# Kernel optimization log

Hardware: AMD Instinct MI355X
Metric: run time of the kernel (lower is better)

## Reference

```python
import jax, jax.numpy as jnp
import numpy as np

R = 3            # num_relations
H = 256          # hid_dim
N0, N1, N2, N3 = 50000, 10000, 4000, 1024   # sampled node counts per hop
FAN = 16         # in-edges per target node
NB_NODES = 100000


def setup_inputs() -> dict:
    keys = iter(jax.random.split(jax.random.key(0), 80))
    def nrm(shape, scale=1.0):
        return jax.random.normal(next(keys), shape, jnp.float32) * scale
    inp = {}
    inp["features"] = nrm((NB_NODES, H))
    inp["n_ids"] = jax.random.randint(next(keys), (R, N0), 0, NB_NODES)
    def edges(n_src, n_dst):
        src = jax.random.randint(next(keys), (R, n_dst * FAN), 0, n_src)
        dst = jnp.tile(jnp.repeat(jnp.arange(n_dst), FAN)[None, :], (R, 1))
        return src, dst
    inp["src1"], inp["dst1"] = edges(N0, N1)
    inp["src2"], inp["dst2"] = edges(N1, N2)
    inp["src3"], inp["dst3"] = edges(N2, N3)
    def tconv_params(p, din, heads, ch):
        hc = heads * ch
        s = 1.0 / np.sqrt(din)
        for nm in ("Wq", "Wk", "Wv", "Ws"):
            inp[p + nm] = nrm((R, din, hc), s)
        for nm in ("bq", "bk", "bv", "bs"):
            inp[p + nm] = jnp.zeros((R, hc), jnp.float32)
        inp[p + "Wb"] = nrm((R, 3 * hc, 1), 1.0 / np.sqrt(3 * hc))
    tconv_params("l1_", H, 2, H // 2)
    tconv_params("l2_", H, 1, H // 2)
    tconv_params("l3_", H // 2, 1, H)
    inp["w_omega"] = nrm((H, H), 1.0 / np.sqrt(H))
    inp["b_omega"] = jnp.zeros((H,), jnp.float32)
    inp["u_omega"] = nrm((H,), 1.0 / np.sqrt(H))
    inp["rl"] = jnp.ones((R, 1), jnp.float32)
    return inp


def _tconv(x, src, dst, n_dst, P, heads, ch):
    """PyG TransformerConv with beta=True (gated skip), concat heads, eval mode."""
    Wq, bq, Wk, bk, Wv, bv, Ws, bs, Wb = P
    x_dst = x[:n_dst]
    q = (x_dst @ Wq + bq).reshape(n_dst, heads, ch)
    k = (x @ Wk + bk).reshape(-1, heads, ch)
    v = (x @ Wv + bv).reshape(-1, heads, ch)
    logit = (q[dst] * k[src]).sum(-1) * (1.0 / np.sqrt(ch))        # [E, heads]
    m = jax.ops.segment_max(logit, dst, num_segments=n_dst)
    p = jnp.exp(logit - m[dst])
    z = jax.ops.segment_sum(p, dst, num_segments=n_dst)
    a = p / z[dst]                                                  # edge softmax
    out = jax.ops.segment_sum(v[src] * a[..., None], dst, num_segments=n_dst)
    out = out.reshape(n_dst, heads * ch)
    x_r = x_dst @ Ws + bs
    g = jax.nn.sigmoid(jnp.concatenate([out, x_r, out - x_r], -1) @ Wb)
    return g * x_r + (1.0 - g) * out


def _rel_forward(feats, n_id, s1, d1, s2, d2, s3, d3, P1, P2, P3):
    x = feats[n_id]                                     # [N0, H]
    x = _tconv(x, s1, d1, N1, P1, 2, H // 2)            # [N1, H]
    x = (x - x.mean(0)) / jnp.sqrt(x.var(0) + 1e-5)     # BatchNorm1d (batch stats, identity affine)
    x = jax.nn.elu(x)
    x = _tconv(x, s2, d2, N2, P2, 1, H // 2)            # [N2, H/2]
    x = _tconv(x, s3, d3, N3, P3, 1, H)                 # [N3, H]
    return x


def _forward(features, n_ids, src1, dst1, src2, dst2, src3, dst3,
             l1_Wq, l1_bq, l1_Wk, l1_bk, l1_Wv, l1_bv, l1_Ws, l1_bs, l1_Wb,
             l2_Wq, l2_bq, l2_Wk, l2_bk, l2_Wv, l2_bv, l2_Ws, l2_bs, l2_Wb,
             l3_Wq, l3_bq, l3_Wk, l3_bk, l3_Wv, l3_bv, l3_Ws, l3_bs, l3_Wb,
             w_omega, b_omega, u_omega, rl):
    P1 = (l1_Wq, l1_bq, l1_Wk, l1_bk, l1_Wv, l1_bv, l1_Ws, l1_bs, l1_Wb)
    P2 = (l2_Wq, l2_bq, l2_Wk, l2_bk, l2_Wv, l2_bv, l2_Ws, l2_bs, l2_Wb)
    P3 = (l3_Wq, l3_bq, l3_Wk, l3_bk, l3_Wv, l3_bv, l3_Ws, l3_bs, l3_Wb)
    per_rel = jax.vmap(_rel_forward, in_axes=(None, 0, 0, 0, 0, 0, 0, 0, 0, 0, 0))
    emb = per_rel(features, n_ids, src1, dst1, src2, dst2, src3, dst3, P1, P2, P3)  # [R, N3, H]
    multi = emb.transpose(1, 0, 2) * rl[None]            # [N3, R, H], RL-threshold scaled
    v = jnp.tanh(multi @ w_omega + b_omega)              # [N3, R, H]
    alphas = jax.nn.softmax(v @ u_omega, axis=1)         # [N3, R]
    return (multi * alphas[..., None]).sum(1)            # [N3, H]


def reference(features, n_ids, src1, dst1, src2, dst2, src3, dst3,
              l1_Wq, l1_bq, l1_Wk, l1_bk, l1_Wv, l1_bv, l1_Ws, l1_bs, l1_Wb,
              l2_Wq, l2_bq, l2_Wk, l2_bk, l2_Wv, l2_bv, l2_Ws, l2_bs, l2_Wb,
              l3_Wq, l3_bq, l3_Wk, l3_bk, l3_Wv, l3_bv, l3_Ws, l3_bs, l3_Wb,
              w_omega, b_omega, u_omega, rl):
    return _forward(features, n_ids, src1, dst1, src2, dst2, src3, dst3,
                    l1_Wq, l1_bq, l1_Wk, l1_bk, l1_Wv, l1_bv, l1_Ws, l1_bs, l1_Wb,
                    l2_Wq, l2_bq, l2_Wk, l2_bk, l2_Wv, l2_bv, l2_Ws, l2_bs, l2_Wb,
                    l3_Wq, l3_bq, l3_Wk, l3_bk, l3_Wv, l3_bv, l3_Ws, l3_bs, l3_Wb,
                    w_omega, b_omega, u_omega, rl)
```

## Files before the change

kernel.cpp:

```cpp
#include <hip/hip_runtime.h>
#include <hip/hip_bf16.h>
#include <math.h>

#define H 256
#define N0 50000
#define N1 10000
#define N2 4000
#define N3 1024
#define FAN 16

typedef __hip_bfloat16 bf16;
typedef __attribute__((ext_vector_type(8))) short short8;
typedef __attribute__((ext_vector_type(4))) short short4v;
typedef __attribute__((ext_vector_type(2))) short short2v;
typedef __attribute__((ext_vector_type(4))) float floatx4;

typedef const __attribute__((address_space(1))) void* gas_ptr;
typedef __attribute__((address_space(3))) void* las_ptr;

__device__ __forceinline__ void load_lds16(const void* g, void* l) {
    __builtin_amdgcn_global_load_lds((gas_ptr)g, (las_ptr)l, 16, 0, 0);
}

__device__ __forceinline__ float2 cvt_bf2(unsigned u) {
    union { unsigned q; float f; } lo, hi;
    lo.q = u << 16; hi.q = u & 0xffff0000u;
    return make_float2(lo.f, hi.f);
}

template<int K>
__global__ __launch_bounds__(256, 4) void gemm_dual(
    const bf16* __restrict__ A, size_t Astr,
    const bf16* __restrict__ BtKV, const bf16* __restrict__ BtQS,
    const float* __restrict__ bk, const float* __restrict__ bv,
    const float* __restrict__ bq, const float* __restrict__ bs, int Nh,
    bf16* __restrict__ Ckv, size_t CkvStr, int Mkv,
    float* __restrict__ Cqs, size_t CqsStr, int Mqs,
    int nbKV)
{
    constexpr int KC = K / 32;
    constexpr int CPR = K / 8;
    constexpr int LOG_CPR = (K == 256) ? 5 : 4;
    constexpr int RPI = 64 / CPR;
    constexpr int ISSUES = 16 / RPI;
    const int N = 2 * Nh;
    __shared__ bf16 A_s[64 * K];

    const int z = blockIdx.z;
    const bool isKV = (int)blockIdx.x < nbKV;
    const int bx = isKV ? blockIdx.x : blockIdx.x - nbKV;
    const int M = isKV ? Mkv : Mqs;
    const bf16* Bt = (isKV ? BtKV : BtQS) + (size_t)z * N * K;
    const float* b1 = (isKV ? bk : bq) + (size_t)z * Nh;
    const float* b2 = (isKV ? bv : bs) + (size_t)z * Nh;
    A += (size_t)z * Astr;

    const int lane = threadIdx.x & 63;
    const int w = threadIdx.x >> 6;
    const int lm = lane & 15;
    const int q = lane >> 4;
    const int mbase = bx * 64;
    const int n0 = blockIdx.y * 256;

    {
        const int ch = lane & (CPR - 1);
        const int rsub = lane >> LOG_CPR;
        #pragma unroll
        for (int i = 0; i < ISSUES; i++) {
            int row = w * 16 + i * RPI + rsub;
            int grow = mbase + row; grow = grow < M ? grow : M - 1;
            int gch = ch ^ (row & 7);
            load_lds16(A + (size_t)grow * K + gch * 8,
                       A_s + (size_t)(w * 16 + i * RPI) * K);
        }
    }

    const bf16* bp[4];
    #pragma unroll
    for (int ni = 0; ni < 4; ni++)
        bp[ni] = Bt + (size_t)(n0 + w * 64 + ni * 16 + lm) * K + q * 8;

    floatx4 acc[4][4];
    #pragma unroll
    for (int i = 0; i < 4; i++)
        #pragma unroll
        for (int j = 0; j < 4; j++)
            acc[i][j] = (floatx4){0.f, 0.f, 0.f, 0.f};

    __syncthreads();

    short8 bn[4];
    #pragma unroll
    for (int ni = 0; ni < 4; ni++) bn[ni] = *(const short8*)(bp[ni]);

    #pragma unroll
    for (int kc = 0; kc < KC; kc++) {
        short8 bc[4];
        #pragma unroll
        for (int ni = 0; ni < 4; ni++) bc[ni] = bn[ni];
        if (kc + 1 < KC) {
            #pragma unroll
            for (int ni = 0; ni < 4; ni++)
                bn[ni] = *(const short8*)(bp[ni] + (kc + 1) * 32);
        }
        short8 af[4];
        #pragma unroll
        for (int mi = 0; mi < 4; mi++) {
            int row = mi * 16 + lm;
            af[mi] = *(const short8*)(A_s + row * K + (((kc * 4 + q) ^ (lm & 7)) * 8));
        }
        #pragma unroll
        for (int mi = 0; mi < 4; mi++)
            #pragma unroll
            for (int ni = 0; ni < 4; ni++)
                acc[mi][ni] = __builtin_amdgcn_mfma_f32_16x16x32_bf16(
                    af[mi], bc[ni], acc[mi][ni], 0, 0, 0);
    }

    if (isKV) {
        bf16* C = Ckv + (size_t)z * CkvStr;
        __syncthreads();
        bf16* stg = A_s + (size_t)w * (16 * 72);
        #pragma unroll
        for (int p = 0; p < 4; p++) {
            #pragma unroll
            for (int ni = 0; ni < 4; ni++) {
                int colg = n0 + w * 64 + ni * 16 + lm;
                float bias = (colg < Nh) ? b1[colg] : b2[colg - Nh];
                #pragma unroll
                for (int rg = 0; rg < 4; rg++)
                    stg[(q * 4 + rg) * 72 + ni * 16 + lm] = (bf16)(acc[p][ni][rg] + bias);
            }
            #pragma unroll
            for (int it = 0; it < 2; it++) {
                int rl = it * 8 + (lane >> 3);
                int grow = mbase + p * 16 + rl;
                short8 vv = *(const short8*)(stg + rl * 72 + (lane & 7) * 8);
                if (grow < M)
                    *(short8*)(C + (size_t)grow * N + n0 + w * 64 + (lane & 7) * 8) = vv;
            }
        }
    } else {
        float* C = Cqs + (size_t)z * CqsStr;
        #pragma unroll
        for (int ni = 0; ni < 4; ni++) {
            int colg = n0 + w * 64 + ni * 16 + lm;
            float bias = (colg < Nh) ? b1[colg] : b2[colg - Nh];
            #pragma unroll
            for (int mi = 0; mi < 4; mi++) {
                int rb = mbase + mi * 16 + q * 4;
                #pragma unroll
                for (int rg = 0; rg < 4; rg++) {
                    int rr = rb + rg;
                    if (rr < M) C[(size_t)rr * N + colg] = acc[mi][ni][rg] + bias;
                }
            }
        }
    }
}

__global__ __launch_bounds__(256) void gather_bf16(
    const float* __restrict__ F, const int* __restrict__ n_ids, bf16* __restrict__ out,
    int nrows)
{
    int z = blockIdx.y;
    const int* idx = n_ids + (size_t)z * nrows;
    bf16* o = out + (size_t)z * nrows * H;
    int t = blockIdx.x * 256 + threadIdx.x;
    int row = t >> 6;
    if (row >= nrows) return;
    int c4 = (t & 63) * 4;
    float4 v = *(const float4*)(F + (size_t)idx[row] * H + c4);
    bf16 tmp[4] = {(bf16)v.x, (bf16)v.y, (bf16)v.z, (bf16)v.w};
    *(short4v*)(o + (size_t)row * H + c4) = *(const short4v*)tmp;
}

__global__ __launch_bounds__(256) void pack_all(
    const float* __restrict__ l1_Wk, const float* __restrict__ l1_Wv,
    const float* __restrict__ l1_Wq, const float* __restrict__ l1_Ws,
    const float* __restrict__ l2_Wk, const float* __restrict__ l2_Wv,
    const float* __restrict__ l2_Wq, const float* __restrict__ l2_Ws,
    const float* __restrict__ l3_Wk, const float* __restrict__ l3_Wv,
    const float* __restrict__ l3_Wq, const float* __restrict__ l3_Ws,
    bf16* __restrict__ Wkv1, bf16* __restrict__ Wqs1,
    bf16* __restrict__ Wkv2, bf16* __restrict__ Wqs2,
    bf16* __restrict__ Wkv3, bf16* __restrict__ Wqs3)
{
    int job = blockIdx.z, r = blockIdx.y, nn = blockIdx.x, k = threadIdx.x;
    const float *W1, *W2; bf16* Wt; int K, Nh;
    switch (job) {
        case 0: W1 = l1_Wk; W2 = l1_Wv; Wt = Wkv1; K = 256; Nh = 256; break;
        case 1: W1 = l1_Wq; W2 = l1_Ws; Wt = Wqs1; K = 256; Nh = 256; break;
        case 2: W1 = l2_Wk; W2 = l2_Wv; Wt = Wkv2; K = 256; Nh = 128; break;
        case 3: W1 = l2_Wq; W2 = l2_Ws; Wt = Wqs2; K = 256; Nh = 128; break;
        case 4: W1 = l3_Wk; W2 = l3_Wv; Wt = Wkv3; K = 128; Nh = 256; break;
        default: W1 = l3_Wq; W2 = l3_Ws; Wt = Wqs3; K = 128; Nh = 256; break;
    }
    if (nn >= 2 * Nh || k >= K) return;
    size_t wstride = (size_t)K * Nh;
    float v = (nn < Nh) ? W1[(size_t)r * wstride + (size_t)k * Nh + nn]
                        : W2[(size_t)r * wstride + (size_t)k * Nh + (nn - Nh)];
    Wt[(size_t)r * 2 * wstride + (size_t)nn * K + k] = (bf16)v;
}

template<int CPL, int HEADS>
__global__ __launch_bounds__(256) void attn_gate(
    const float* __restrict__ qs, size_t qsStr,
    const bf16* __restrict__ kv, size_t kvStr,
    const int* __restrict__ src,
    const float* __restrict__ Wb,
    float* __restrict__ yf, size_t yfStr,
    bf16* __restrict__ yb, size_t ybStr,
    int ndst, float scale)
{
    constexpr int hc = CPL * 64;
    constexpr int LPH = 64 / HEADS;
    const int z = blockIdx.y;
    int lane = threadIdx.x & 63;
    int d = blockIdx.x * 4 + (threadIdx.x >> 6);
    if (d >= ndst) return;
    qs += (size_t)z * qsStr;
    kv += (size_t)z * kvStr;
    src += (size_t)z * ndst * FAN;
    Wb += (size_t)z * 3 * hc;

    const float* qp = qs + (size_t)d * (2 * hc) + lane * CPL;
    float qv[CPL], xv[CPL];
    if constexpr (CPL == 2) {
        float2 a = *(const float2*)qp;
        float2 b = *(const float2*)(qp + hc);
        qv[0] = a.x; qv[1] = a.y; xv[0] = b.x; xv[1] = b.y;
    } else {
        float4 a = *(const float4*)qp;
        float4 b = *(const float4*)(qp + hc);
        qv[0] = a.x; qv[1] = a.y; qv[2] = a.z; qv[3] = a.w;
        xv[0] = b.x; xv[1] = b.y; xv[2] = b.z; xv[3] = b.w;
    }
    const int* sp = src + (size_t)d * FAN;
    int sidx[FAN];
    #pragma unroll
    for (int e = 0; e < FAN; e++) sidx[e] = sp[e];

    float part[FAN];
    #pragma unroll
    for (int e = 0; e < FAN; e++) {
        const bf16* kp = kv + (size_t)sidx[e] * (2 * hc) + lane * CPL;
        if constexpr (CPL == 2) {
            float2 kf = cvt_bf2(*(const unsigned*)kp);
            part[e] = qv[0] * kf.x + qv[1] * kf.y;
        } else {
            uint2 u = *(const uint2*)kp;
            float2 k0 = cvt_bf2(u.x), k1 = cvt_bf2(u.y);
            part[e] = qv[0] * k0.x + qv[1] * k0.y + qv[2] * k1.x + qv[3] * k1.y;
        }
    }
    float logit[FAN], mx = -1e30f;
    #pragma unroll
    for (int e = 0; e < FAN; e++) {
        float dt = part[e];
        #pragma unroll
        for (int off = LPH / 2; off > 0; off >>= 1) dt += __shfl_xor(dt, off, 64);
        dt *= scale;
        logit[e] = dt;
        mx = fmaxf(mx, dt);
    }
    float zsum = 0.f, p[FAN];
    #pragma unroll
    for (int e = 0; e < FAN; e++) { p[e] = __expf(logit[e] - mx); zsum += p[e]; }
    float inv = 1.f / zsum;

    float ov[CPL];
    #pragma unroll
    for (int j = 0; j < CPL; j++) ov[j] = 0.f;
    #pragma unroll
    for (int e = 0; e < FAN; e++) {
        const bf16* vp = kv + (size_t)sidx[e] * (2 * hc) + hc + lane * CPL;
        if constexpr (CPL == 2) {
            float2 vf = cvt_bf2(*(const unsigned*)vp);
            ov[0] += p[e] * vf.x; ov[1] += p[e] * vf.y;
        } else {
            uint2 u = *(const uint2*)vp;
            float2 v0 = cvt_bf2(u.x), v1 = cvt_bf2(u.y);
            ov[0] += p[e] * v0.x; ov[1] += p[e] * v0.y;
            ov[2] += p[e] * v1.x; ov[3] += p[e] * v1.y;
        }
    }
    #pragma unroll
    for (int j = 0; j < CPL; j++) ov[j] *= inv;

    float s = 0.f;
    #pragma unroll
    for (int j = 0; j < CPL; j++) {
        int c = lane * CPL + j;
        s += ov[j] * Wb[c] + xv[j] * Wb[hc + c] + (ov[j] - xv[j]) * Wb[2 * hc + c];
    }
    #pragma unroll
    for (int off = 32; off > 0; off >>= 1) s += __shfl_xor(s, off, 64);
    float g = 1.f / (1.f + __expf(-s));

    float yv[CPL];
    #pragma unroll
    for (int j = 0; j < CPL; j++) yv[j] = g * xv[j] + (1.f - g) * ov[j];

    if (yf) {
        float* op = yf + (size_t)z * yfStr + (size_t)d * hc + lane * CPL;
        if constexpr (CPL == 2) *(float2*)op = make_float2(yv[0], yv[1]);
        else *(float4*)op = make_float4(yv[0], yv[1], yv[2], yv[3]);
    }
    if (yb) {
        bf16* op = yb + (size_t)z * ybStr + (size_t)d * hc + lane * CPL;
        bf16 tmp[CPL];
        #pragma unroll
        for (int j = 0; j < CPL; j++) tmp[j] = (bf16)yv[j];
        if constexpr (CPL == 2) *(short2v*)op = *(const short2v*)tmp;
        else *(short4v*)op = *(const short4v*)tmp;
    }
}

__global__ __launch_bounds__(256) void colstat_partial(
    const bf16* __restrict__ x, size_t xStr, int M,
    float* __restrict__ ps, float* __restrict__ pss)
{
    int z = blockIdx.y;
    const bf16* xp = x + (size_t)z * xStr;
    int f = threadIdx.x;
    int b = blockIdx.x;
    float s = 0.f, ss = 0.f;
    for (int r = b; r < M; r += 64) {
        float v = (float)xp[(size_t)r * H + f];
        s += v; ss += v * v;
    }
    ps[((size_t)z * 64 + b) * H + f] = s;
    pss[((size_t)z * 64 + b) * H + f] = ss;
}

__global__ __launch_bounds__(256) void colfinal_norm_elu(
    const float* __restrict__ ps, const float* __restrict__ pss,
    bf16* __restrict__ x, size_t xStr, int M)
{
    int z = blockIdx.y;
    bf16* xp = x + (size_t)z * xStr;
    int c = threadIdx.x;
    float s = 0.f, ss = 0.f;
    #pragma unroll 8
    for (int b = 0; b < 64; b++) {
        s += ps[((size_t)z * 64 + b) * H + c];
        ss += pss[((size_t)z * 64 + b) * H + c];
    }
    float mu = s / M;
    float istd = rsqrtf(ss / M - mu * mu + 1e-5f);
    for (int r = blockIdx.x; r < M; r += gridDim.x) {
        float t = ((float)xp[(size_t)r * H + c] - mu) * istd;
        xp[(size_t)r * H + c] = (bf16)(t > 0.f ? t : __expf(t) - 1.0f);
    }
}

__global__ __launch_bounds__(256) void semantic_kernel(
    const float* __restrict__ emb,
    const float* __restrict__ Wo, const float* __restrict__ bo,
    const float* __restrict__ uo, const float* __restrict__ rl,
    float* __restrict__ outp)
{
    __shared__ float m_s[3][H];
    __shared__ float red[H];
    __shared__ float score_s[3];
    int n = blockIdx.x, c = threadIdx.x;
    for (int r = 0; r < 3; r++)
        m_s[r][c] = emb[((size_t)r * N3 + n) * H + c] * rl[r];
    __syncthreads();
    for (int r = 0; r < 3; r++) {
        float t = bo[c];
        for (int k2 = 0; k2 < H; k2++) t += m_s[r][k2] * Wo[k2 * H + c];
        red[c] = tanhf(t) * uo[c];
        __syncthreads();
        for (int s = 128; s > 0; s >>= 1) {
            if (c < s) red[c] += red[c + s];
            __syncthreads();
        }
        if (c == 0) score_s[r] = red[0];
        __syncthreads();
    }
    float s0 = score_s[0], s1 = score_s[1], s2 = score_s[2];
    float mx = fmaxf(s0, fmaxf(s1, s2));
    float e0 = __expf(s0 - mx), e1 = __expf(s1 - mx), e2 = __expf(s2 - mx);
    float zi = 1.0f / (e0 + e1 + e2);
    outp[(size_t)n * H + c] = (m_s[0][c] * e0 + m_s[1][c] * e1 + m_s[2][c] * e2) * zi;
}

extern "C" void kernel_launch(void* const* d_in, const int* in_sizes, int n_in,
                              void* d_out, int out_size, void* d_ws, size_t ws_size,
                              hipStream_t stream) {
    const float* features = (const float*)d_in[0];
    const int*   n_ids    = (const int*)d_in[1];
    const int*   src1     = (const int*)d_in[2];
    const int*   src2     = (const int*)d_in[4];
    const int*   src3     = (const int*)d_in[6];
    const float* l1_Wq = (const float*)d_in[8];
    const float* l1_Wk = (const float*)d_in[9];
    const float* l1_Wv = (const float*)d_in[10];
    const float* l1_Ws = (const float*)d_in[11];
    const float* l1_bq = (const float*)d_in[12];
    const float* l1_bk = (const float*)d_in[13];
    const float* l1_bv = (const float*)d_in[14];
    const float* l1_bs = (const float*)d_in[15];
    const float* l1_Wb = (const float*)d_in[16];
    const float* l2_Wq = (const float*)d_in[17];
    const float* l2_Wk = (const float*)d_in[18];
    const float* l2_Wv = (const float*)d_in[19];
    const float* l2_Ws = (const float*)d_in[20];
    const float* l2_bq = (const float*)d_in[21];
    const float* l2_bk = (const float*)d_in[22];
    const float* l2_bv = (const float*)d_in[23];
    const float* l2_bs = (const float*)d_in[24];
    const float* l2_Wb = (const float*)d_in[25];
    const float* l3_Wq = (const float*)d_in[26];
    const float* l3_Wk = (const float*)d_in[27];
    const float* l3_Wv = (const float*)d_in[28];
    const float* l3_Ws = (const float*)d_in[29];
    const float* l3_bq = (const float*)d_in[30];
    const float* l3_bk = (const float*)d_in[31];
    const float* l3_bv = (const float*)d_in[32];
    const float* l3_bs = (const float*)d_in[33];
    const float* l3_Wb = (const float*)d_in[34];
    const float* w_omega = (const float*)d_in[35];
    const float* b_omega = (const float*)d_in[36];
    const float* u_omega = (const float*)d_in[37];
    const float* rl      = (const float*)d_in[38];

    float* ws = (float*)d_ws;
    size_t o = 0;
    float* emb = ws + o; o += (size_t)3 * N3 * H;
    float* qs1 = ws + o; o += (size_t)3 * N1 * 512;
    float* qs2 = ws + o; o += (size_t)3 * N2 * 256;
    float* qs3 = ws + o; o += (size_t)3 * N3 * 512;
    float* ps  = ws + o; o += (size_t)3 * 64 * H;
    float* pss = ws + o; o += (size_t)3 * 64 * H;

    bf16* bws = (bf16*)(ws + o);
    size_t b = 0;
    bf16* Xg  = bws + b; b += (size_t)3 * N0 * H;
    bf16* kv1 = bws + b; b += (size_t)3 * N0 * 512;
    bf16* x1b = bws + b; b += (size_t)3 * N1 * 256;
    bf16* kv2 = bws + b; b += (size_t)3 * N1 * 256;
    bf16* x2b = bws + b; b += (size_t)3 * N2 * 128;
    bf16* kv3 = bws + b; b += (size_t)3 * N2 * 512;
    bf16* Wkv1 = bws + b; b += (size_t)3 * 512 * H;
    bf16* Wqs1 = bws + b; b += (size_t)3 * 512 * H;
    bf16* Wkv2 = bws + b; b += (size_t)3 * 256 * H;
    bf16* Wqs2 = bws + b; b += (size_t)3 * 256 * H;
    bf16* Wkv3 = bws + b; b += (size_t)3 * 512 * 128;
    bf16* Wqs3 = bws + b; b += (size_t)3 * 512 * 128;

    const float sc128 = 0.088388347648318447f;
    const float sc256 = 0.0625f;

    pack_all<<<dim3(512, 3, 6), 256, 0, stream>>>(
        l1_Wk, l1_Wv, l1_Wq, l1_Ws, l2_Wk, l2_Wv, l2_Wq, l2_Ws,
        l3_Wk, l3_Wv, l3_Wq, l3_Ws, Wkv1, Wqs1, Wkv2, Wqs2, Wkv3, Wqs3);

    gather_bf16<<<dim3((N0 * 64 + 255) / 256, 3), 256, 0, stream>>>(
        features, n_ids, Xg, N0);

    {
        int nbKV = (N0 + 63) / 64, nbQS = (N1 + 63) / 64;
        gemm_dual<256><<<dim3(nbKV + nbQS, 2, 3), 256, 0, stream>>>(
            Xg, (size_t)N0 * H, Wkv1, Wqs1, l1_bk, l1_bv, l1_bq, l1_bs, 256,
            kv1, (size_t)N0 * 512, N0, qs1, (size_t)N1 * 512, N1, nbKV);
    }
    attn_gate<4, 2><<<dim3((N1 + 3) / 4, 3), 256, 0, stream>>>(
        qs1, (size_t)N1 * 512, kv1, (size_t)N0 * 512, src1, l1_Wb,
        (float*)nullptr, 0, x1b, (size_t)N1 * 256, N1, sc128);
    colstat_partial<<<dim3(64, 3), 256, 0, stream>>>(x1b, (size_t)N1 * 256, N1, ps, pss);
    colfinal_norm_elu<<<dim3(128, 3), 256, 0, stream>>>(ps, pss, x1b, (size_t)N1 * 256, N1);

    {
        int nbKV = (N1 + 63) / 64, nbQS = (N2 + 63) / 64;
        gemm_dual<256><<<dim3(nbKV + nbQS, 1, 3), 256, 0, stream>>>(
            x1b, (size_t)N1 * 256, Wkv2, Wqs2, l2_bk, l2_bv, l2_bq, l2_bs, 128,
            kv2, (size_t)N1 * 256, N1, qs2, (size_t)N2 * 256, N2, nbKV);
    }
    attn_gate<2, 1><<<dim3((N2 + 3) / 4, 3), 256, 0, stream>>>(
        qs2, (size_t)N2 * 256, kv2, (size_t)N1 * 256, src2, l2_Wb,
        (float*)nullptr, 0, x2b, (size_t)N2 * 128, N2, sc128);

    {
        int nbKV = (N2 + 63) / 64, nbQS = (N3 + 63) / 64;
        gemm_dual<128><<<dim3(nbKV + nbQS, 2, 3), 256, 0, stream>>>(
            x2b, (size_t)N2 * 128, Wkv3, Wqs3, l3_bk, l3_bv, l3_bq, l3_bs, 256,
            kv3, (size_t)N2 * 512, N2, qs3, (size_t)N3 * 512, N3, nbKV);
    }
    attn_gate<4, 1><<<dim3((N3 + 3) / 4, 3), 256, 0, stream>>>(
        qs3, (size_t)N3 * 512, kv3, (size_t)N2 * 512, src3, l3_Wb,
        emb, (size_t)N3 * H, (bf16*)nullptr, 0, N3, sc256);

    semantic_kernel<<<N3, 256, 0, stream>>>(emb, w_omega, b_omega, u_omega, rl, (float*)d_out);
}
```

Baseline: 614.7 us.

## Make dual GEMM persistent with double-buffered LDS prefetch of next A tile

The dual K/V and Q/S projection GEMM becomes a persistent kernel: a capped grid walks over row tiles in a stride loop, and the async global-to-LDS load of the next A tile is issued into a second LDS buffer while the current tile is computed. B fragments are also prefetched two k-steps ahead instead of one. The goal is to hide A-tile load latency and per-block launch and ramp-up cost. In exchange, LDS use doubles, the occupancy hint drops from 4 to 2 blocks per unit, and register pressure rises.

Result: no change. 613.0 us (-0.3%).

```diff
diff --git a/kernel.cpp b/kernel.cpp
--- a/kernel.cpp
+++ b/kernel.cpp
@@ -29,14 +29,14 @@
 }
 
 template<int K>
-__global__ __launch_bounds__(256, 4) void gemm_dual(
+__global__ __launch_bounds__(256, 2) void gemm_dual(
     const bf16* __restrict__ A, size_t Astr,
     const bf16* __restrict__ BtKV, const bf16* __restrict__ BtQS,
     const float* __restrict__ bk, const float* __restrict__ bv,
     const float* __restrict__ bq, const float* __restrict__ bs, int Nh,
     bf16* __restrict__ Ckv, size_t CkvStr, int Mkv,
     float* __restrict__ Cqs, size_t CqsStr, int Mqs,
-    int nbKV)
+    int nbKV, int nbTot)
 {
     constexpr int KC = K / 32;
     constexpr int CPR = K / 8;
@@ -44,115 +44,134 @@
     constexpr int RPI = 64 / CPR;
     constexpr int ISSUES = 16 / RPI;
     const int N = 2 * Nh;
-    __shared__ bf16 A_s[64 * K];
+    __shared__ bf16 A_s[2][64 * K];
 
     const int z = blockIdx.z;
-    const bool isKV = (int)blockIdx.x < nbKV;
-    const int bx = isKV ? blockIdx.x : blockIdx.x - nbKV;
-    const int M = isKV ? Mkv : Mqs;
-    const bf16* Bt = (isKV ? BtKV : BtQS) + (size_t)z * N * K;
-    const float* b1 = (isKV ? bk : bq) + (size_t)z * Nh;
-    const float* b2 = (isKV ? bv : bs) + (size_t)z * Nh;
     A += (size_t)z * Astr;
 
     const int lane = threadIdx.x & 63;
     const int w = threadIdx.x >> 6;
     const int lm = lane & 15;
     const int q = lane >> 4;
-    const int mbase = bx * 64;
     const int n0 = blockIdx.y * 256;
 
-    {
-        const int ch = lane & (CPR - 1);
-        const int rsub = lane >> LOG_CPR;
+    const int ch = lane & (CPR - 1);
+    const int rsub = lane >> LOG_CPR;
+
+    auto stage = [&](int bx, bf16* dst) {
+        const bool iskv = bx < nbKV;
+        const int M = iskv ? Mkv : Mqs;
+        const int mb = (iskv ? bx : bx - nbKV) * 64;
         #pragma unroll
         for (int i = 0; i < ISSUES; i++) {
             int row = w * 16 + i * RPI + rsub;
-            int grow = mbase + row; grow = grow < M ? grow : M - 1;
+            int grow = mb + row; grow = grow < M ? grow : M - 1;
             int gch = ch ^ (row & 7);
             load_lds16(A + (size_t)grow * K + gch * 8,
-                       A_s + (size_t)(w * 16 + i * RPI) * K);
-        }
-    }
-
-    const bf16* bp[4];
-    #pragma unroll
-    for (int ni = 0; ni < 4; ni++)
-        bp[ni] = Bt + (size_t)(n0 + w * 64 + ni * 16 + lm) * K + q * 8;
-
-    floatx4 acc[4][4];
-    #pragma unroll
-    for (int i = 0; i < 4; i++)
-        #pragma unroll
-        for (int j = 0; j < 4; j++)
-            acc[i][j] = (floatx4){0.f, 0.f, 0.f, 0.f};
-
-    __syncthreads();
-
-    short8 bn[4];
-    #pragma unroll
-    for (int ni = 0; ni < 4; ni++) bn[ni] = *(const short8*)(bp[ni]);
-
-    #pragma unroll
-    for (int kc = 0; kc < KC; kc++) {
-        short8 bc[4];
-        #pragma unroll
-        for (int ni = 0; ni < 4; ni++) bc[ni] = bn[ni];
-        if (kc + 1 < KC) {
+                       dst + (size_t)(w * 16 + i * RPI) * K);
+        }
+    };
+
+    const int bx0 = blockIdx.x;
+    if (bx0 >= nbTot) return;
+    stage(bx0, A_s[0]);
+
+    int cur = 0;
+    for (int bx = bx0; bx < nbTot; bx += gridDim.x, cur ^= 1) {
+        const bool isKV = bx < nbKV;
+        const int bxr = isKV ? bx : bx - nbKV;
+        const int M = isKV ? Mkv : Mqs;
+        const int mbase = bxr * 64;
+        const bf16* Bt = (isKV ? BtKV : BtQS) + (size_t)z * N * K;
+        const float* b1 = (isKV ? bk : bq) + (size_t)z * Nh;
+        const float* b2 = (isKV ? bv : bs) + (size_t)z * Nh;
+
+        const bf16* bp[4];
+        #pragma unroll
+        for (int ni = 0; ni < 4; ni++)
+            bp[ni] = Bt + (size_t)(n0 + w * 64 + ni * 16 + lm) * K + q * 8;
+
+        floatx4 acc[4][4];
+        #pragma unroll
+        for (int i = 0; i < 4; i++)
             #pragma unroll
-            for (int ni = 0; ni < 4; ni++)
-                bn[ni] = *(const short8*)(bp[ni] + (kc + 1) * 32);
-        }
-        short8 af[4];
-        #pragma unroll
-        for (int mi = 0; mi < 4; mi++) {
-            int row = mi * 16 + lm;
-            af[mi] = *(const short8*)(A_s + row * K + (((kc * 4 + q) ^ (lm & 7)) * 8));
-        }
-        #pragma unroll
-        for (int mi = 0; mi < 4; mi++)
+            for (int j = 0; j < 4; j++)
+                acc[i][j] = (floatx4){0.f, 0.f, 0.f, 0.f};
+
+        __syncthreads();
+
+        short8 bn[4], bn2[4];
+        #pragma unroll
+        for (int ni = 0; ni < 4; ni++) bn[ni] = *(const short8*)(bp[ni]);
+        #pragma unroll
+        for (int ni = 0; ni < 4; ni++) bn2[ni] = *(const short8*)(bp[ni] + 32);
+        {
+            int nxt = bx + gridDim.x;
+            if (nxt < nbTot) stage(nxt, A_s[cur ^ 1]);
+        }
+
+        const bf16* As = A_s[cur];
+        #pragma unroll
+        for (int kc = 0; kc < KC; kc++) {
+            short8 bc[4];
             #pragma unroll
-            for (int ni = 0; ni < 4; ni++)
-                acc[mi][ni] = __builtin_amdgcn_mfma_f32_16x16x32_bf16(
-                    af[mi], bc[ni], acc[mi][ni], 0, 0, 0);
-    }
-
-    if (isKV) {
-        bf16* C = Ckv + (size_t)z * CkvStr;
-        __syncthreads();
-        bf16* stg = A_s + (size_t)w * (16 * 72);
-        #pragma unroll
-        for (int p = 0; p < 4; p++) {
+            for (int ni = 0; ni < 4; ni++) { bc[ni] = bn[ni]; bn[ni] = bn2[ni]; }
+            if (kc + 2 < KC) {
+                #pragma unroll
+                for (int ni = 0; ni < 4; ni++)
+                    bn2[ni] = *(const short8*)(bp[ni] + (kc + 2) * 32);
+            }
+            short8 af[4];
+            #pragma unroll
+            for (int mi = 0; mi < 4; mi++) {
+                int row = mi * 16 + lm;
+                af[mi] = *(const short8*)(As + row * K + (((kc * 4 + q) ^ (lm & 7)) * 8));
+            }
+            #pragma unroll
+            for (int mi = 0; mi < 4; mi++)
+                #pragma unroll
+                for (int ni = 0; ni < 4; ni++)
+                    acc[mi][ni] = __builtin_amdgcn_mfma_f32_16x16x32_bf16(
+                        af[mi], bc[ni], acc[mi][ni], 0, 0, 0);
+        }
+
+        if (isKV) {
+            bf16* C = Ckv + (size_t)z * CkvStr;
+            __syncthreads();
+            bf16* stg = A_s[cur] + (size_t)w * (16 * 72);
+            #pragma unroll
+            for (int p = 0; p < 4; p++) {
+                #pragma unroll
+                for (int ni = 0; ni < 4; ni++) {
+                    int colg = n0 + w * 64 + ni * 16 + lm;
+                    float bias = (colg < Nh) ? b1[colg] : b2[colg - Nh];
+                    #pragma unroll
+                    for (int rg = 0; rg < 4; rg++)
+                        stg[(q * 4 + rg) * 72 + ni * 16 + lm] = (bf16)(acc[p][ni][rg] + bias);
+                }
+                #pragma unroll
+                for (int it = 0; it < 2; it++) {
+                    int rl = it * 8 + (lane >> 3);
+                    int grow = mbase + p * 16 + rl;
+                    short8 vv = *(const short8*)(stg + rl * 72 + (lane & 7) * 8);
+                    if (grow < M)
+                        *(short8*)(C + (size_t)grow * N + n0 + w * 64 + (lane & 7) * 8) = vv;
+                }
+            }
+        } else {
+            float* C = Cqs + (size_t)z * CqsStr;
             #pragma unroll
             for (int ni = 0; ni < 4; ni++) {
                 int colg = n0 + w * 64 + ni * 16 + lm;
                 float bias = (colg < Nh) ? b1[colg] : b2[colg - Nh];
                 #pragma unroll
-                for (int rg = 0; rg < 4; rg++)
-                    stg[(q * 4 + rg) * 72 + ni * 16 + lm] = (bf16)(acc[p][ni][rg] + bias);
-            }
-            #pragma unroll
-            for (int it = 0; it < 2; it++) {
-                int rl = it * 8 + (lane >> 3);
-                int grow = mbase + p * 16 + rl;
-                short8 vv = *(const short8*)(stg + rl * 72 + (lane & 7) * 8);
-                if (grow < M)
-                    *(short8*)(C + (size_t)grow * N + n0 + w * 64 + (lane & 7) * 8) = vv;
-            }
-        }
-    } else {
-        float* C = Cqs + (size_t)z * CqsStr;
-        #pragma unroll
-        for (int ni = 0; ni < 4; ni++) {
-            int colg = n0 + w * 64 + ni * 16 + lm;
-            float bias = (colg < Nh) ? b1[colg] : b2[colg - Nh];
-            #pragma unroll
-            for (int mi = 0; mi < 4; mi++) {
-                int rb = mbase + mi * 16 + q * 4;
-                #pragma unroll
-                for (int rg = 0; rg < 4; rg++) {
-                    int rr = rb + rg;
-                    if (rr < M) C[(size_t)rr * N + colg] = acc[mi][ni][rg] + bias;
+                for (int mi = 0; mi < 4; mi++) {
+                    int rb = mbase + mi * 16 + q * 4;
+                    #pragma unroll
+                    for (int rg = 0; rg < 4; rg++) {
+                        int rr = rb + rg;
+                        if (rr < M) C[(size_t)rr * N + colg] = acc[mi][ni][rg] + bias;
+                    }
                 }
             }
         }
@@ -462,10 +481,11 @@
         features, n_ids, Xg, N0);
 
     {
-        int nbKV = (N0 + 63) / 64, nbQS = (N1 + 63) / 64;
-        gemm_dual<256><<<dim3(nbKV + nbQS, 2, 3), 256, 0, stream>>>(
+        int nbKV = (N0 + 63) / 64, nbQS = (N1 + 63) / 64, nbTot = nbKV + nbQS;
+        int gx = 512 / 6; if (gx > nbTot) gx = nbTot;
+        gemm_dual<256><<<dim3(gx, 2, 3), 256, 0, stream>>>(
             Xg, (size_t)N0 * H, Wkv1, Wqs1, l1_bk, l1_bv, l1_bq, l1_bs, 256,
-            kv1, (size_t)N0 * 512, N0, qs1, (size_t)N1 * 512, N1, nbKV);
+            kv1, (size_t)N0 * 512, N0, qs1, (size_t)N1 * 512, N1, nbKV, nbTot);
     }
     attn_gate<4, 2><<<dim3((N1 + 3) / 4, 3), 256, 0, stream>>>(
         qs1, (size_t)N1 * 512, kv1, (size_t)N0 * 512, src1, l1_Wb,
@@ -474,20 +494,22 @@
     colfinal_norm_elu<<<dim3(128, 3), 256, 0, stream>>>(ps, pss, x1b, (size_t)N1 * 256, N1);
 
     {
-        int nbKV = (N1 + 63) / 64, nbQS = (N2 + 63) / 64;
-        gemm_dual<256><<<dim3(nbKV + nbQS, 1, 3), 256, 0, stream>>>(
+        int nbKV = (N1 + 63) / 64, nbQS = (N2 + 63) / 64, nbTot = nbKV + nbQS;
+        int gx = 512 / 3; if (gx > nbTot) gx = nbTot;
+        gemm_dual<256><<<dim3(gx, 1, 3), 256, 0, stream>>>(
             x1b, (size_t)N1 * 256, Wkv2, Wqs2, l2_bk, l2_bv, l2_bq, l2_bs, 128,
-            kv2, (size_t)N1 * 256, N1, qs2, (size_t)N2 * 256, N2, nbKV);
+            kv2, (size_t)N1 * 256, N1, qs2, (size_t)N2 * 256, N2, nbKV, nbTot);
     }
     attn_gate<2, 1><<<dim3((N2 + 3) / 4, 3), 256, 0, stream>>>(
         qs2, (size_t)N2 * 256, kv2, (size_t)N1 * 256, src2, l2_Wb,
         (float*)nullptr, 0, x2b, (size_t)N2 * 128, N2, sc128);
 
     {
-        int nbKV = (N2 + 63) / 64, nbQS = (N3 + 63) / 64;
-        gemm_dual<128><<<dim3(nbKV + nbQS, 2, 3), 256, 0, stream>>>(
+        int nbKV = (N2 + 63) / 64, nbQS = (N3 + 63) / 64, nbTot = nbKV + nbQS;
+        int gx = 512 / 6; if (gx > nbTot) gx = nbTot;
+        gemm_dual<128><<<dim3(gx, 2, 3), 256, 0, stream>>>(
             x2b, (size_t)N2 * 128, Wkv3, Wqs3, l3_bk, l3_bv, l3_bq, l3_bs, 256,
-            kv3, (size_t)N2 * 512, N2, qs3, (size_t)N3 * 512, N3, nbKV);
+            kv3, (size_t)N2 * 512, N2, qs3, (size_t)N3 * 512, N3, nbKV, nbTot);
     }
     attn_gate<4, 1><<<dim3((N3 + 3) / 4, 3), 256, 0, stream>>>(
         qs3, (size_t)N3 * 512, kv3, (size_t)N2 * 512, src3, l3_Wb,
```
